# Kernel optimization log

Measured on AMD Instinct MI355X. Metric: run time of the kernel, lower is better.

The kernel has to match this reference:

```python
import jax, jax.numpy as jnp
import numpy as np

V, D, C, L, F = 32000, 1024, 2048, 6, 4096
B, S = 2, 2048


def _layer_norm(x, w, b, eps=1e-5):
    mu = jnp.mean(x, axis=-1, keepdims=True)
    var = jnp.mean(jnp.square(x - mu), axis=-1, keepdims=True)
    return (x - mu) * jax.lax.rsqrt(var + eps) * w + b


def setup_inputs() -> dict:
    key = jax.random.key(0)
    ks = jax.random.split(key, 16)
    s = 0.02
    inp = {
        "tokens": jax.random.randint(ks[0], (B, S), 0, V),
        "embed_table": jax.random.normal(ks[1], (V, D), jnp.float32) * s,
        "pos_table": jax.random.normal(ks[2], (C, D), jnp.float32) * s,
        # stacked per-layer params [L, ...]
        "ln1_w": jnp.ones((L, D), jnp.float32),
        "ln1_b": jnp.zeros((L, D), jnp.float32),
        "qkv_w": jax.random.normal(ks[3], (L, 3 * D, D), jnp.float32) * s,
        "qkv_b": jnp.zeros((L, 3 * D), jnp.float32),
        "ln2_w": jnp.ones((L, D), jnp.float32),
        "ln2_b": jnp.zeros((L, D), jnp.float32),
        "ffa_w": jax.random.normal(ks[4], (L, F, D), jnp.float32) * s,
        "ffa_b": jnp.zeros((L, F), jnp.float32),
        "ffb_w": jax.random.normal(ks[5], (L, D, F), jnp.float32) * s,
        "ffb_b": jnp.zeros((L, D), jnp.float32),
        "out_w": jax.random.normal(ks[6], (V, D), jnp.float32) * s,
    }
    return inp


def _forward(tokens, embed_table, pos_table, ln1_w, ln1_b, qkv_w, qkv_b,
             ln2_w, ln2_b, ffa_w, ffa_b, ffb_w, ffb_b, out_w):
    Sx = tokens.shape[1]
    h = embed_table[tokens] + pos_table[:Sx][None, :, :]  # [B,S,D]
    causal = jnp.triu(jnp.ones((Sx, Sx), bool), k=1)       # True = masked
    scale = jnp.float32(D) ** 0.5

    def block(h, p):
        l1w, l1b, qw, qb, l2w, l2b, aw, ab, bw, bb = p
        a = _layer_norm(h, l1w, l1b)
        qkv = jnp.einsum('bsd,ed->bse', a, qw) + qb       # [B,S,3D]
        q, k, v = jnp.split(qkv, 3, axis=-1)
        scores = jnp.einsum('bsd,btd->bst', q, k)          # [B,S,S]
        scores = jnp.where(causal[None], -jnp.inf, scores)
        attn = jax.nn.softmax(scores / scale, axis=-1)
        h = h + jnp.einsum('bst,btd->bsd', attn, v)
        f = _layer_norm(h, l2w, l2b)
        f = jax.nn.relu(jnp.einsum('bsd,fd->bsf', f, aw) + ab)
        h = h + jnp.einsum('bsf,df->bsd', f, bw) + bb
        return h, None

    params = (ln1_w, ln1_b, qkv_w, qkv_b, ln2_w, ln2_b, ffa_w, ffa_b, ffb_w, ffb_b)
    h, _ = jax.lax.scan(block, h, params)
    # OutputLayer applies only the Linear (output_norm is defined but unused)
    return jnp.einsum('bsd,vd->bsv', h, out_w)


def reference(tokens, embed_table, pos_table, ln1_w, ln1_b, qkv_w, qkv_b,
              ln2_w, ln2_b, ffa_w, ffa_b, ffb_w, ffb_b, out_w):
    return _forward(tokens, embed_table, pos_table, ln1_w, ln1_b, qkv_w, qkv_b,
                    ln2_w, ln2_b, ffa_w, ffa_b, ffb_w, ffb_b, out_w)
```

## Files before the change

kernel.cpp:

```cpp
#include <hip/hip_runtime.h>

#define Dm 1024
#define Sm 2048
#define Bm 2
#define Lm 6
#define Fm 4096
#define Vm 32000
#define MT (Bm*Sm)

typedef unsigned short u16;
typedef unsigned int   u32;
typedef __attribute__((ext_vector_type(8))) short bf16x8;
typedef __attribute__((ext_vector_type(4))) float f32x4;

__device__ __forceinline__ u16 f2bf(float f) {
  u32 u = __float_as_uint(f);
  u += 0x7fffu + ((u >> 16) & 1u);
  return (u16)(u >> 16);
}
__device__ __forceinline__ u32 pack2(float a, float b) {
  return (u32)f2bf(a) | ((u32)f2bf(b) << 16);
}
__device__ __forceinline__ void gload16(const void* g, void* l) {
  __builtin_amdgcn_global_load_lds(
      (const __attribute__((address_space(1))) void*)g,
      (__attribute__((address_space(3))) void*)l, 16, 0, 0);
}

__global__ __launch_bounds__(256) void embed_kernel(
    const int* __restrict__ tok, const float* __restrict__ emb,
    const float* __restrict__ pos, float* __restrict__ h)
{
  int i  = blockIdx.x * 256 + threadIdx.x;
  int d  = (i & (Dm/4 - 1)) * 4;
  int bs = i >> 8;
  int s  = bs & (Sm - 1);
  int t  = tok[bs];
  float4 e = *(const float4*)(emb + (size_t)t * Dm + d);
  float4 p = *(const float4*)(pos + (size_t)s * Dm + d);
  float4 r; r.x = e.x + p.x; r.y = e.y + p.y; r.z = e.z + p.z; r.w = e.w + p.w;
  *(float4*)(h + (size_t)bs * Dm + d) = r;
}

__global__ __launch_bounds__(256) void ln_kernel(
    const float* __restrict__ x, const float* __restrict__ w,
    const float* __restrict__ b, u16* __restrict__ o)
{
  __shared__ float red[8];
  int row = blockIdx.x, tid = threadIdx.x;
  const float* xr = x + (size_t)row * Dm;
  float4 v = *(const float4*)(xr + tid * 4);
  float s1 = v.x + v.y + v.z + v.w;
  float s2 = v.x*v.x + v.y*v.y + v.z*v.z + v.w*v.w;
  #pragma unroll
  for (int off = 32; off; off >>= 1) {
    s1 += __shfl_down(s1, off, 64);
    s2 += __shfl_down(s2, off, 64);
  }
  int lane = tid & 63, wv = tid >> 6;
  if (!lane) { red[wv] = s1; red[4 + wv] = s2; }
  __syncthreads();
  s1 = red[0] + red[1] + red[2] + red[3];
  s2 = red[4] + red[5] + red[6] + red[7];
  float mu = s1 * (1.f / Dm);
  float rs = rsqrtf(s2 * (1.f / Dm) - mu * mu + 1e-5f);
  float4 wv4 = *(const float4*)(w + tid * 4);
  float4 bv4 = *(const float4*)(b + tid * 4);
  uint2 pk;
  pk.x = pack2((v.x - mu) * rs * wv4.x + bv4.x, (v.y - mu) * rs * wv4.y + bv4.y);
  pk.y = pack2((v.z - mu) * rs * wv4.z + bv4.z, (v.w - mu) * rs * wv4.w + bv4.w);
  *(uint2*)(o + (size_t)row * Dm + tid * 4) = pk;
}

__global__ __launch_bounds__(256) void softmax_kernel(
    const float* __restrict__ sc, u16* __restrict__ at)
{
  __shared__ float red[8];
  int gr = blockIdx.x;
  int s  = gr & (Sm - 1);
  const float* x = sc + (size_t)gr * Sm;
  u16* o = at + (size_t)gr * Sm;
  int tid = threadIdx.x;
  float4 v0 = *(const float4*)(x + tid * 8);
  float4 v1 = *(const float4*)(x + tid * 8 + 4);
  float vals[8] = {v0.x, v0.y, v0.z, v0.w, v1.x, v1.y, v1.z, v1.w};
  float mx = -1e30f;
  #pragma unroll
  for (int j = 0; j < 8; ++j) {
    int t = tid * 8 + j;
    vals[j] = (t <= s) ? vals[j] * 0.03125f : -1e30f;
    mx = fmaxf(mx, vals[j]);
  }
  #pragma unroll
  for (int off = 32; off; off >>= 1) mx = fmaxf(mx, __shfl_down(mx, off, 64));
  int lane = tid & 63, wv = tid >> 6;
  if (!lane) red[wv] = mx;
  __syncthreads();
  mx = fmaxf(fmaxf(red[0], red[1]), fmaxf(red[2], red[3]));
  __syncthreads();
  float e[8], sm = 0.f;
  #pragma unroll
  for (int j = 0; j < 8; ++j) {
    int t = tid * 8 + j;
    e[j] = (t <= s) ? __expf(vals[j] - mx) : 0.f;
    sm += e[j];
  }
  #pragma unroll
  for (int off = 32; off; off >>= 1) sm += __shfl_down(sm, off, 64);
  if (!lane) red[wv] = sm;
  __syncthreads();
  sm = red[0] + red[1] + red[2] + red[3];
  float inv = 1.f / sm;
  uint4 p;
  p.x = pack2(e[0]*inv, e[1]*inv); p.y = pack2(e[2]*inv, e[3]*inv);
  p.z = pack2(e[4]*inv, e[5]*inv); p.w = pack2(e[6]*inv, e[7]*inv);
  *(uint4*)(o + tid * 8) = p;
}

__global__ __launch_bounds__(256) void cvt8_kernel(
    const float* __restrict__ x, u16* __restrict__ o)
{
  size_t i = ((size_t)blockIdx.x * 256 + threadIdx.x) * 8;
  float4 v0 = *(const float4*)(x + i);
  float4 v1 = *(const float4*)(x + i + 4);
  uint4 p; p.x = pack2(v0.x, v0.y); p.y = pack2(v0.z, v0.w);
  p.z = pack2(v1.x, v1.y); p.w = pack2(v1.z, v1.w);
  *(uint4*)(o + i) = p;
}

__global__ __launch_bounds__(256) void cvtw_kernel(
    const float* __restrict__ qw, const float* __restrict__ aw,
    const float* __restrict__ bw, u16* __restrict__ o)
{
  int b = blockIdx.x;
  const float* src; u16* dst; int idx;
  if (b < 1536)      { src = qw; dst = o;                     idx = b; }
  else if (b < 3584) { src = aw; dst = o + 3*Dm*Dm;           idx = b - 1536; }
  else               { src = bw; dst = o + 3*Dm*Dm + Fm*Dm;   idx = b - 3584; }
  size_t i = ((size_t)idx * 256 + threadIdx.x) * 8;
  float4 v0 = *(const float4*)(src + i);
  float4 v1 = *(const float4*)(src + i + 4);
  uint4 p; p.x = pack2(v0.x, v0.y); p.y = pack2(v0.z, v0.w);
  p.z = pack2(v1.x, v1.y); p.w = pack2(v1.z, v1.w);
  *(uint4*)(dst + i) = p;
}

__global__ __launch_bounds__(256) void vtr_kernel(
    const u16* __restrict__ v, u16* __restrict__ vT)
{
  __shared__ u16 t[64][64];
  int b = blockIdx.z;
  int s0 = blockIdx.x * 64, d0 = blockIdx.y * 64;
  const u16* src = v + ((size_t)b * Sm + s0) * (3 * Dm) + d0;
  int tid = threadIdx.x;
  int rr = tid >> 3, cc = (tid & 7) * 8;
  #pragma unroll
  for (int it = 0; it < 2; ++it) {
    int r = rr + it * 32;
    uint4 x = *(const uint4*)(src + (size_t)r * (3 * Dm) + cc);
    *(uint4*)&t[r][cc ^ (((r >> 3) & 7) << 3)] = x;
  }
  __syncthreads();
  u16* dst = vT + ((size_t)b * Dm + d0) * Sm + s0;
  #pragma unroll
  for (int it = 0; it < 2; ++it) {
    int d = rr + it * 32;
    u16 tmp[8];
    #pragma unroll
    for (int j = 0; j < 8; ++j) {
      int r = cc + j;
      tmp[j] = t[r][d ^ (((r >> 3) & 7) << 3)];
    }
    *(uint4*)(dst + (size_t)d * Sm + cc) = *(uint4*)tmp;
  }
}

enum { EPI_F32 = 0, EPI_BF16 = 1, EPI_RELU_BF16 = 2, EPI_RES = 3, EPI_F32NT = 4 };

__global__ __launch_bounds__(256, 2)
void gemm_kernel(const u16* __restrict__ A, const u16* __restrict__ B,
                 float* __restrict__ outF, u16* __restrict__ outB,
                 const float* __restrict__ bias, const float* __restrict__ resid,
                 int N, int K, int lda, int ldb,
                 long sA, long sB, long sO, long sR,
                 int mshift, int epi, int swz, int cmode)
{
  __shared__ __align__(16) short As[128 * 64];
  __shared__ __align__(16) short Bs[128 * 64];

  const int z = blockIdx.z;
  int bid = blockIdx.x;
  if (swz) { int cpx = gridDim.x >> 3; bid = (bid & 7) * cpx + (bid >> 3); }
  const int m0 = (bid & ((1 << mshift) - 1)) << 7;
  const int n0 = (bid >> mshift) << 7;

  if (cmode == 1 && n0 > m0) return;
  const int keff = (cmode == 2) ? min(K, m0 + 128) : K;

  const u16* Az = A + (size_t)z * sA;
  const u16* Bz = B + (size_t)z * sB;

  const int tid = threadIdx.x;
  const int l   = tid & 63;
  const int w   = tid >> 6;
  const int sub = l >> 3;
  const int colb = ((l & 7) ^ sub) << 4;
  const int row0 = w * 32 + sub;

  const char* gA = (const char*)(Az + (size_t)(m0 + row0) * lda) + colb;
  const char* gB = (const char*)(Bz + (size_t)(n0 + row0) * ldb) + colb;
  const size_t stepA = (size_t)8 * lda * 2;
  const size_t stepB = (size_t)8 * ldb * 2;
  char* lA = (char*)As + w * 4096;
  char* lB = (char*)Bs + w * 4096;

  const int wm   = (w >> 1) * 64;
  const int wn   = (w & 1) * 64;
  const int lrow = l & 15;
  const int kgrp = l >> 4;

  f32x4 acc[4][4];
  #pragma unroll
  for (int i = 0; i < 4; ++i)
    #pragma unroll
    for (int j = 0; j < 4; ++j)
      acc[i][j] = (f32x4){0.f, 0.f, 0.f, 0.f};

  for (int k0 = 0; k0 < keff; k0 += 64) {
    __syncthreads();
    const char* ga = gA + (size_t)k0 * 2;
    const char* gb = gB + (size_t)k0 * 2;
    #pragma unroll
    for (int c = 0; c < 4; ++c) {
      gload16(ga + c * stepA, lA + c * 1024);
      gload16(gb + c * stepB, lB + c * 1024);
    }
    __syncthreads();
    #pragma unroll
    for (int kk = 0; kk < 2; ++kk) {
      bf16x8 af[4], bf_[4];
      #pragma unroll
      for (int i = 0; i < 4; ++i) {
        int ar = wm + i * 16 + lrow;
        af[i]  = *(const bf16x8*)((const char*)As + ar * 128 +
                                  ((kk * 64 + kgrp * 16) ^ ((ar & 7) << 4)));
        int br = wn + i * 16 + lrow;
        bf_[i] = *(const bf16x8*)((const char*)Bs + br * 128 +
                                  ((kk * 64 + kgrp * 16) ^ ((br & 7) << 4)));
      }
      #pragma unroll
      for (int i = 0; i < 4; ++i)
        #pragma unroll
        for (int j = 0; j < 4; ++j)
          acc[i][j] = __builtin_amdgcn_mfma_f32_16x16x32_bf16(af[i], bf_[j], acc[i][j], 0, 0, 0);
    }
  }

  #pragma unroll
  for (int i = 0; i < 4; ++i) {
    #pragma unroll
    for (int j = 0; j < 4; ++j) {
      #pragma unroll
      for (int r = 0; r < 4; ++r) {
        int m = m0 + wm + i * 16 + kgrp * 4 + r;
        int n = n0 + wn + j * 16 + lrow;
        float v = acc[i][j][r];
        if (bias) v += bias[n];
        if (epi == EPI_F32) {
          outF[(size_t)z * sO + (size_t)m * N + n] = v;
        } else if (epi == EPI_BF16) {
          outB[(size_t)m * N + n] = f2bf(v);
        } else if (epi == EPI_RELU_BF16) {
          outB[(size_t)m * N + n] = f2bf(fmaxf(v, 0.f));
        } else {
          float* o = outF + (size_t)z * sO;
          const float* rsd = resid + (size_t)z * sR;
          o[(size_t)m * N + n] = rsd[(size_t)m * N + n] + v;
        }
      }
    }
  }
}

#define BAR_IN()  { __builtin_amdgcn_s_barrier(); \
                    asm volatile("s_waitcnt lgkmcnt(0)" ::: "memory"); \
                    __builtin_amdgcn_sched_barrier(0); \
                    __builtin_amdgcn_s_setprio(1); }
#define BAR_OUT() { __builtin_amdgcn_s_setprio(0); \
                    __builtin_amdgcn_sched_barrier(0); \
                    __builtin_amdgcn_s_barrier(); }

__global__ __launch_bounds__(512, 2)
void gemm256_kernel(const u16* __restrict__ A, const u16* __restrict__ B,
                    float* __restrict__ outF, u16* __restrict__ outB,
                    const float* __restrict__ bias,
                    int N, int K, int mshift, int epi)
{
  extern __shared__ char lds[];

  int bid = blockIdx.x;
  { int cpx = gridDim.x >> 3; bid = (bid & 7) * cpx + (bid >> 3); }
  const int m0 = (bid & ((1 << mshift) - 1)) << 8;
  const int n0 = (bid >> mshift) << 8;

  const int tid = threadIdx.x;
  const int l = tid & 63, w = tid >> 6;
  const int wr = w >> 2, wc = w & 3;
  const int lrow = l & 15, kgrp = l >> 4;
  const int wrbase = wr * 128, wcbase = wc * 64;
  const int srow = (w << 3) + (l >> 3);
  const int scol = ((l & 7) ^ (l >> 3)) << 3;
  const int nt = K >> 6;

  f32x4 acc[8][4];
  #pragma unroll
  for (int i = 0; i < 8; ++i)
    #pragma unroll
    for (int j = 0; j < 4; ++j)
      acc[i][j] = (f32x4){0.f, 0.f, 0.f, 0.f};

  auto STG = [&](int slot, const u16* gb, int grow0, int kel) {
    const u16* g = gb + (size_t)(grow0 + srow) * K + kel + scol;
    gload16(g, lds + slot + w * 1024);
    gload16(g + (size_t)64 * K, lds + slot + 8192 + w * 1024);
  };

  STG(0,              A, m0,       0);
  STG(16384,          A, m0 + 128, 0);
  STG(32768,          B, n0,       0);
  STG(49152,          B, n0 + 128, 0);
  STG(65536 + 32768,  B, n0,       64);
  STG(65536 + 49152,  B, n0 + 128, 64);
  STG(65536,          A, m0,       64);
  asm volatile("s_waitcnt vmcnt(6)" ::: "memory");
  __builtin_amdgcn_s_barrier();

  bf16x8 af[4][2], bfr[4][2];

  #define RDA(base, q) { _Pragma("unroll") \
    for (int f2 = 0; f2 < 4; ++f2) { _Pragma("unroll") \
      for (int kk = 0; kk < 2; ++kk) { \
        int row = wrbase + (q) * 64 + f2 * 16 + lrow; \
        af[f2][kk] = *(const bf16x8*)((base) + row * 128 + \
                       ((kk * 64 + kgrp * 16) ^ ((row & 7) << 4))); } } }
  #define RDB(base, h) { _Pragma("unroll") \
    for (int j2 = 0; j2 < 2; ++j2) { _Pragma("unroll") \
      for (int kk = 0; kk < 2; ++kk) { \
        int row = wcbase + ((h) * 2 + j2) * 16 + lrow; \
        bfr[(h) * 2 + j2][kk] = *(const bf16x8*)((base) + row * 128 + \
                       ((kk * 64 + kgrp * 16) ^ ((row & 7) << 4))); } } }
  #define MM(fi0, fj0) { _Pragma("unroll") \
    for (int f2 = 0; f2 < 4; ++f2) { _Pragma("unroll") \
      for (int j2 = 0; j2 < 2; ++j2) { _Pragma("unroll") \
        for (int kk = 0; kk < 2; ++kk) \
          acc[(fi0) + f2][(fj0) + j2] = __builtin_amdgcn_mfma_f32_16x16x32_bf16( \
              af[f2][kk], bfr[(fj0) + j2][kk], acc[(fi0) + f2][(fj0) + j2], 0, 0, 0); } } }

  const char* c0A = lds;
  const char* c0B = lds + 32768;
  const char* c1A = lds + 65536;
  const char* c1B = lds + 65536 + 32768;

  for (int i = 0; i < (nt >> 1) - 1; ++i) {
    const int kA1 = (2 * i + 1) << 6;
    const int kN0 = (2 * i + 2) << 6;
    const int kN1 = (2 * i + 3) << 6;
    RDA(c0A, 0); RDB(c0B, 0);
    STG(65536 + 16384, A, m0 + 128, kA1);
    BAR_IN(); MM(0, 0); BAR_OUT();
    RDB(c0B, 1);
    BAR_IN(); MM(0, 2); BAR_OUT();
    RDA(c0A, 1);
    STG(32768, B, n0, kN0);
    BAR_IN(); MM(4, 0); BAR_OUT();
    STG(49152, B, n0 + 128, kN0);
    STG(0,     A, m0,       kN0);
    STG(16384, A, m0 + 128, kN0);
    BAR_IN(); MM(4, 2);
    __builtin_amdgcn_s_setprio(0);
    __builtin_amdgcn_sched_barrier(0);
    asm volatile("s_waitcnt vmcnt(8)" ::: "memory");
    __builtin_amdgcn_s_barrier();
    RDA(c1A, 0); RDB(c1B, 0);
    BAR_IN(); MM(0, 0); BAR_OUT();
    RDB(c1B, 1);
    BAR_IN(); MM(0, 2); BAR_OUT();
    RDA(c1A, 1);
    STG(65536 + 32768, B, n0, kN1);
    BAR_IN(); MM(4, 0); BAR_OUT();
    STG(65536 + 49152, B, n0 + 128, kN1);
    STG(65536,         A, m0,       kN1);
    BAR_IN(); MM(4, 2);
    __builtin_amdgcn_s_setprio(0);
    __builtin_amdgcn_sched_barrier(0);
    asm volatile("s_waitcnt vmcnt(6)" ::: "memory");
    __builtin_amdgcn_s_barrier();
  }

  {
    RDA(c0A, 0); RDB(c0B, 0);
    STG(65536 + 16384, A, m0 + 128, (nt - 1) << 6);
    BAR_IN(); MM(0, 0); BAR_OUT();
    RDB(c0B, 1);
    BAR_IN(); MM(0, 2); BAR_OUT();
    RDA(c0A, 1);
    BAR_IN(); MM(4, 0); BAR_OUT();
    BAR_IN(); MM(4, 2);
    __builtin_amdgcn_s_setprio(0);
    __builtin_amdgcn_sched_barrier(0);
    asm volatile("s_waitcnt vmcnt(0)" ::: "memory");
    __builtin_amdgcn_s_barrier();
    RDA(c1A, 0); RDB(c1B, 0);
    BAR_IN(); MM(0, 0); BAR_OUT();
    RDB(c1B, 1);
    BAR_IN(); MM(0, 2); BAR_OUT();
    RDA(c1A, 1);
    BAR_IN(); MM(4, 0); BAR_OUT();
    BAR_IN(); MM(4, 2);
    __builtin_amdgcn_s_setprio(0);
  }

  #pragma unroll
  for (int fi = 0; fi < 8; ++fi) {
    #pragma unroll
    for (int fj = 0; fj < 4; ++fj) {
      #pragma unroll
      for (int r = 0; r < 4; ++r) {
        int m = m0 + wrbase + fi * 16 + kgrp * 4 + r;
        int n = n0 + wcbase + fj * 16 + lrow;
        float v = acc[fi][fj][r];
        if (bias) v += bias[n];
        if (epi == EPI_F32) {
          outF[(size_t)m * N + n] = v;
        } else if (epi == EPI_F32NT) {
          __builtin_nontemporal_store(v, outF + (size_t)m * N + n);
        } else if (epi == EPI_BF16) {
          outB[(size_t)m * N + n] = f2bf(v);
        } else {
          outB[(size_t)m * N + n] = f2bf(fmaxf(v, 0.f));
        }
      }
    }
  }
}

extern "C" void kernel_launch(void* const* d_in, const int* in_sizes, int n_in,
                              void* d_out, int out_size, void* d_ws, size_t ws_size,
                              hipStream_t stream)
{
  const int*   tok  = (const int*)d_in[0];
  const float* emb  = (const float*)d_in[1];
  const float* pos  = (const float*)d_in[2];
  const float* ln1w = (const float*)d_in[3];
  const float* ln1b = (const float*)d_in[4];
  const float* qkvw = (const float*)d_in[5];
  const float* qkvb = (const float*)d_in[6];
  const float* ln2w = (const float*)d_in[7];
  const float* ln2b = (const float*)d_in[8];
  const float* ffaw = (const float*)d_in[9];
  const float* ffab = (const float*)d_in[10];
  const float* ffbw = (const float*)d_in[11];
  const float* ffbb = (const float*)d_in[12];
  const float* outw = (const float*)d_in[13];
  float* out = (float*)d_out;

  hipFuncSetAttribute((const void*)gemm256_kernel,
                      hipFuncAttributeMaxDynamicSharedMemorySize, 131072);

  char* p = (char*)d_ws;
  float* h      = (float*)p;  p += (size_t)MT * Dm * 4;
  u16*   a      = (u16*)p;    p += (size_t)MT * Dm * 2;
  u16*   hb     = (u16*)p;    p += (size_t)MT * Dm * 2;
  u16*   qkv    = (u16*)p;    p += (size_t)MT * 3 * Dm * 2;
  u16*   vT     = (u16*)p;    p += (size_t)Bm * Dm * Sm * 2;
  float* scores = (float*)p;  p += (size_t)Bm * Sm * Sm * 4;
  u16*   attn   = (u16*)p;    p += (size_t)Bm * Sm * Sm * 2;
  u16*   f      = (u16*)p;    p += (size_t)MT * Fm * 2;
  u16*   wlb    = (u16*)p;    p += (size_t)(3*Dm*Dm + Fm*Dm + Dm*Fm) * 2;
  u16*   owb    = qkv;

  embed_kernel<<<MT * Dm / 1024, 256, 0, stream>>>(tok, emb, pos, h);

  for (int l = 0; l < Lm; ++l) {
    cvtw_kernel<<<5632, 256, 0, stream>>>(
        qkvw + (size_t)l * 3 * Dm * Dm, ffaw + (size_t)l * Fm * Dm,
        ffbw + (size_t)l * Dm * Fm, wlb);
    ln_kernel<<<MT, 256, 0, stream>>>(h, ln1w + l * Dm, ln1b + l * Dm, a);
    gemm256_kernel<<<dim3(192), 512, 131072, stream>>>(
        a, wlb, nullptr, qkv, qkvb + l * 3 * Dm, 3 * Dm, Dm, 4, EPI_BF16);
    gemm_kernel<<<dim3(256, 1, Bm), 256, 0, stream>>>(
        qkv, qkv + Dm, scores, nullptr, nullptr, nullptr,
        Sm, Dm, 3 * Dm, 3 * Dm, (long)Sm * 3 * Dm, (long)Sm * 3 * Dm,
        (long)Sm * Sm, 0, 4, EPI_F32, 0, 1);
    softmax_kernel<<<Bm * Sm, 256, 0, stream>>>(scores, attn);
    vtr_kernel<<<dim3(32, 16, Bm), 256, 0, stream>>>(qkv + 2 * Dm, vT);
    gemm_kernel<<<dim3(128, 1, Bm), 256, 0, stream>>>(
        attn, vT, h, nullptr, nullptr, h,
        Dm, Sm, Sm, Sm, (long)Sm * Sm, (long)Dm * Sm,
        (long)Sm * Dm, (long)Sm * Dm, 4, EPI_RES, 0, 2);
    ln_kernel<<<MT, 256, 0, stream>>>(h, ln2w + l * Dm, ln2b + l * Dm, a);
    gemm256_kernel<<<dim3(256), 512, 131072, stream>>>(
        a, wlb + 3 * Dm * Dm, nullptr, f, ffab + l * Fm, Fm, Dm, 4, EPI_RELU_BF16);
    gemm_kernel<<<dim3(256, 1, 1), 256, 0, stream>>>(
        f, wlb + 3 * Dm * Dm + Fm * Dm, h, nullptr, ffbb + l * Dm, h,
        Dm, Fm, Fm, Fm, 0, 0, 0, 0, 5, EPI_RES, 1, 0);
  }

  cvt8_kernel<<<MT * Dm / 2048, 256, 0, stream>>>(h, hb);
  cvt8_kernel<<<Vm * Dm / 2048, 256, 0, stream>>>(outw, owb);
  gemm256_kernel<<<dim3(2000), 512, 131072, stream>>>(
      hb, owb, out, nullptr, nullptr, Vm, Dm, 4, EPI_F32NT);
}
```

Measured before the change: 2.338 ms.

## Double-buffer register fragments to overlap LDS reads with MFMA in gemm256

Restructures the 256x256 GEMM main loop so the A and B fragments use separate register sets (aq0/aq1, bh0/bh1). The LDS reads for the next quarter-tile are issued before the current MFMA block, and the old double barrier around each MFMA group becomes a single barrier. The prologue now also prefetches the second A half and the first fragments, and the stage schedule is reshuffled. This is meant to hide LDS read latency and cut barrier count, at the cost of more VGPRs under the 512x2 launch bound and tighter correctness reasoning about buffer reuse.

```diff
diff --git a/kernel.cpp b/kernel.cpp
--- a/kernel.cpp
+++ b/kernel.cpp
@@ -282,13 +282,11 @@
   }
 }
 
-#define BAR_IN()  { __builtin_amdgcn_s_barrier(); \
-                    asm volatile("s_waitcnt lgkmcnt(0)" ::: "memory"); \
-                    __builtin_amdgcn_sched_barrier(0); \
-                    __builtin_amdgcn_s_setprio(1); }
-#define BAR_OUT() { __builtin_amdgcn_s_setprio(0); \
-                    __builtin_amdgcn_sched_barrier(0); \
-                    __builtin_amdgcn_s_barrier(); }
+#define LGKM0() { asm volatile("s_waitcnt lgkmcnt(0)" ::: "memory"); \
+                  __builtin_amdgcn_sched_barrier(0); }
+#define SB()    __builtin_amdgcn_sched_barrier(0)
+#define PRIO_MM(X) { __builtin_amdgcn_s_setprio(1); X; \
+                     __builtin_amdgcn_s_setprio(0); SB(); }
 
 __global__ __launch_bounds__(512, 2)
 void gemm256_kernel(const u16* __restrict__ A, const u16* __restrict__ B,
@@ -312,6 +310,11 @@
   const int scol = ((l & 7) ^ (l >> 3)) << 3;
   const int nt = K >> 6;
 
+  const char* c0A = lds;
+  const char* c0B = lds + 32768;
+  const char* c1A = lds + 65536;
+  const char* c1B = lds + 98304;
+
   f32x4 acc[8][4];
   #pragma unroll
   for (int i = 0; i < 8; ++i)
@@ -325,99 +328,113 @@
     gload16(g + (size_t)64 * K, lds + slot + 8192 + w * 1024);
   };
 
-  STG(0,              A, m0,       0);
-  STG(16384,          A, m0 + 128, 0);
-  STG(32768,          B, n0,       0);
-  STG(49152,          B, n0 + 128, 0);
-  STG(65536 + 32768,  B, n0,       64);
-  STG(65536 + 49152,  B, n0 + 128, 64);
-  STG(65536,          A, m0,       64);
-  asm volatile("s_waitcnt vmcnt(6)" ::: "memory");
-  __builtin_amdgcn_s_barrier();
-
-  bf16x8 af[4][2], bfr[4][2];
-
-  #define RDA(base, q) { _Pragma("unroll") \
+  bf16x8 aq0[4][2], aq1[4][2], bh0[2][2], bh1[2][2];
+
+  #define RD_A(dst, base, q) { _Pragma("unroll") \
     for (int f2 = 0; f2 < 4; ++f2) { _Pragma("unroll") \
       for (int kk = 0; kk < 2; ++kk) { \
         int row = wrbase + (q) * 64 + f2 * 16 + lrow; \
-        af[f2][kk] = *(const bf16x8*)((base) + row * 128 + \
+        dst[f2][kk] = *(const bf16x8*)((base) + row * 128 + \
                        ((kk * 64 + kgrp * 16) ^ ((row & 7) << 4))); } } }
-  #define RDB(base, h) { _Pragma("unroll") \
+  #define RD_B(dst, base, h) { _Pragma("unroll") \
     for (int j2 = 0; j2 < 2; ++j2) { _Pragma("unroll") \
       for (int kk = 0; kk < 2; ++kk) { \
         int row = wcbase + ((h) * 2 + j2) * 16 + lrow; \
-        bfr[(h) * 2 + j2][kk] = *(const bf16x8*)((base) + row * 128 + \
+        dst[j2][kk] = *(const bf16x8*)((base) + row * 128 + \
                        ((kk * 64 + kgrp * 16) ^ ((row & 7) << 4))); } } }
-  #define MM(fi0, fj0) { _Pragma("unroll") \
+  #define MMX(fi0, aa, fj0, bb) { _Pragma("unroll") \
     for (int f2 = 0; f2 < 4; ++f2) { _Pragma("unroll") \
       for (int j2 = 0; j2 < 2; ++j2) { _Pragma("unroll") \
         for (int kk = 0; kk < 2; ++kk) \
           acc[(fi0) + f2][(fj0) + j2] = __builtin_amdgcn_mfma_f32_16x16x32_bf16( \
-              af[f2][kk], bfr[(fj0) + j2][kk], acc[(fi0) + f2][(fj0) + j2], 0, 0, 0); } } }
-
-  const char* c0A = lds;
-  const char* c0B = lds + 32768;
-  const char* c1A = lds + 65536;
-  const char* c1B = lds + 65536 + 32768;
+              aa[f2][kk], bb[j2][kk], acc[(fi0) + f2][(fj0) + j2], 0, 0, 0); } } }
+
+  STG(0,     A, m0,       0);
+  STG(16384, A, m0 + 128, 0);
+  STG(32768, B, n0,       0);
+  STG(49152, B, n0 + 128, 0);
+  STG(65536 + 32768, B, n0,       64);
+  STG(65536 + 49152, B, n0 + 128, 64);
+  STG(65536,         A, m0,       64);
+  STG(65536 + 16384, A, m0 + 128, 64);
+  asm volatile("s_waitcnt vmcnt(8)" ::: "memory");
+  __builtin_amdgcn_s_barrier();
+  RD_A(aq0, c0A, 0); RD_B(bh0, c0B, 0);
 
   for (int i = 0; i < (nt >> 1) - 1; ++i) {
-    const int kA1 = (2 * i + 1) << 6;
     const int kN0 = (2 * i + 2) << 6;
     const int kN1 = (2 * i + 3) << 6;
-    RDA(c0A, 0); RDB(c0B, 0);
-    STG(65536 + 16384, A, m0 + 128, kA1);
-    BAR_IN(); MM(0, 0); BAR_OUT();
-    RDB(c0B, 1);
-    BAR_IN(); MM(0, 2); BAR_OUT();
-    RDA(c0A, 1);
+    LGKM0();
+    RD_B(bh1, c0B, 1); SB();
+    PRIO_MM(MMX(0, aq0, 0, bh0));
+    __builtin_amdgcn_s_barrier();
+    LGKM0();
     STG(32768, B, n0, kN0);
-    BAR_IN(); MM(4, 0); BAR_OUT();
-    STG(49152, B, n0 + 128, kN0);
+    RD_A(aq1, c0A, 1); SB();
+    PRIO_MM(MMX(0, aq0, 2, bh1));
+    __builtin_amdgcn_s_barrier();
+    LGKM0();
+    STG(49152, B, n0 + 128, kN0); SB();
+    PRIO_MM(MMX(4, aq1, 0, bh0));
+    __builtin_amdgcn_s_barrier();
+    LGKM0();
     STG(0,     A, m0,       kN0);
     STG(16384, A, m0 + 128, kN0);
-    BAR_IN(); MM(4, 2);
-    __builtin_amdgcn_s_setprio(0);
-    __builtin_amdgcn_sched_barrier(0);
     asm volatile("s_waitcnt vmcnt(8)" ::: "memory");
-    __builtin_amdgcn_s_barrier();
-    RDA(c1A, 0); RDB(c1B, 0);
-    BAR_IN(); MM(0, 0); BAR_OUT();
-    RDB(c1B, 1);
-    BAR_IN(); MM(0, 2); BAR_OUT();
-    RDA(c1A, 1);
+    SB();
+    RD_A(aq0, c1A, 0); RD_B(bh0, c1B, 0); SB();
+    PRIO_MM(MMX(4, aq1, 2, bh1));
+    __builtin_amdgcn_s_barrier();
+    LGKM0();
+    RD_B(bh1, c1B, 1); SB();
+    PRIO_MM(MMX(0, aq0, 0, bh0));
+    __builtin_amdgcn_s_barrier();
+    LGKM0();
     STG(65536 + 32768, B, n0, kN1);
-    BAR_IN(); MM(4, 0); BAR_OUT();
-    STG(65536 + 49152, B, n0 + 128, kN1);
+    RD_A(aq1, c1A, 1); SB();
+    PRIO_MM(MMX(0, aq0, 2, bh1));
+    __builtin_amdgcn_s_barrier();
+    LGKM0();
+    STG(65536 + 49152, B, n0 + 128, kN1); SB();
+    PRIO_MM(MMX(4, aq1, 0, bh0));
+    __builtin_amdgcn_s_barrier();
+    LGKM0();
     STG(65536,         A, m0,       kN1);
-    BAR_IN(); MM(4, 2);
-    __builtin_amdgcn_s_setprio(0);
-    __builtin_amdgcn_sched_barrier(0);
-    asm volatile("s_waitcnt vmcnt(6)" ::: "memory");
+    STG(65536 + 16384, A, m0 + 128, kN1);
+    asm volatile("s_waitcnt vmcnt(8)" ::: "memory");
+    SB();
+    RD_A(aq0, c0A, 0); RD_B(bh0, c0B, 0); SB();
+    PRIO_MM(MMX(4, aq1, 2, bh1));
     __builtin_amdgcn_s_barrier();
   }
 
   {
-    RDA(c0A, 0); RDB(c0B, 0);
-    STG(65536 + 16384, A, m0 + 128, (nt - 1) << 6);
-    BAR_IN(); MM(0, 0); BAR_OUT();
-    RDB(c0B, 1);
-    BAR_IN(); MM(0, 2); BAR_OUT();
-    RDA(c0A, 1);
-    BAR_IN(); MM(4, 0); BAR_OUT();
-    BAR_IN(); MM(4, 2);
-    __builtin_amdgcn_s_setprio(0);
-    __builtin_amdgcn_sched_barrier(0);
+    LGKM0(); RD_B(bh1, c0B, 1); SB();
+    PRIO_MM(MMX(0, aq0, 0, bh0));
+    __builtin_amdgcn_s_barrier();
+    LGKM0(); RD_A(aq1, c0A, 1); SB();
+    PRIO_MM(MMX(0, aq0, 2, bh1));
+    __builtin_amdgcn_s_barrier();
+    LGKM0(); SB();
+    PRIO_MM(MMX(4, aq1, 0, bh0));
+    __builtin_amdgcn_s_barrier();
+    LGKM0();
     asm volatile("s_waitcnt vmcnt(0)" ::: "memory");
-    __builtin_amdgcn_s_barrier();
-    RDA(c1A, 0); RDB(c1B, 0);
-    BAR_IN(); MM(0, 0); BAR_OUT();
-    RDB(c1B, 1);
-    BAR_IN(); MM(0, 2); BAR_OUT();
-    RDA(c1A, 1);
-    BAR_IN(); MM(4, 0); BAR_OUT();
-    BAR_IN(); MM(4, 2);
-    __builtin_amdgcn_s_setprio(0);
+    SB();
+    RD_A(aq0, c1A, 0); RD_B(bh0, c1B, 0); SB();
+    PRIO_MM(MMX(4, aq1, 2, bh1));
+    __builtin_amdgcn_s_barrier();
+    LGKM0(); RD_B(bh1, c1B, 1); SB();
+    PRIO_MM(MMX(0, aq0, 0, bh0));
+    __builtin_amdgcn_s_barrier();
+    LGKM0(); RD_A(aq1, c1A, 1); SB();
+    PRIO_MM(MMX(0, aq0, 2, bh1));
+    __builtin_amdgcn_s_barrier();
+    LGKM0(); SB();
+    PRIO_MM(MMX(4, aq1, 0, bh0));
+    __builtin_amdgcn_s_barrier();
+    LGKM0(); SB();
+    PRIO_MM(MMX(4, aq1, 2, bh1));
   }
 
   #pragma unroll
```

Result: slower. 4.191 ms (+79.3%).
